# Performance work log

Measured on AMD Instinct MI355X. Metric: run time of the kernel, lower is better.

The kernel has to match this reference:

```python
import jax, jax.numpy as jnp
import numpy as np

B, A, HR = 2, 180, 512
H_OUT = W_OUT = 512


def setup_inputs() -> dict:
    key = jax.random.key(0)
    k1, = jax.random.split(key, 1)
    sino = jax.random.normal(k1, (B, A, HR), dtype=jnp.float32)
    angles_deg = jnp.linspace(0.0, 180.0, A, endpoint=False, dtype=jnp.float32)
    return {"sino": sino, "angles_deg": angles_deg, "H": H_OUT, "W": W_OUT}


def _forward(sino, angles_deg, H, W):
    Bn, An, Hr = sino.shape
    pad = int(1.0 * 0.1 * min(H, W))  # pad_ratio = 1.0
    Hp, Wp = H + 2 * pad, W + 2 * pad

    # --- F.interpolate bilinear, align_corners=False: (A,B,Hr,1) -> (A,B,Hp,Wp).
    # Input width is 1, so width interp replicates the single column; only height interp matters.
    src = jnp.clip((jnp.arange(Hp, dtype=jnp.float32) + 0.5) * (Hr / Hp) - 0.5, 0.0, Hr - 1)
    i0 = jnp.floor(src).astype(jnp.int32)
    i1 = jnp.minimum(i0 + 1, Hr - 1)
    wH = src - i0.astype(jnp.float32)
    p = jnp.transpose(sino, (1, 0, 2)).astype(jnp.float32)  # (A,B,Hr)
    col = p[:, :, i0] * (1.0 - wH) + p[:, :, i1] * wH       # (A,B,Hp)
    proj = jnp.broadcast_to(col[:, :, :, None], (An, Bn, Hp, Wp))  # (A,B,Hp,Wp)

    # --- affine_grid (align_corners=False), sign = -1
    th = -jnp.deg2rad(angles_deg)
    c, s = jnp.cos(th), jnp.sin(th)                          # (A,)
    xs = (jnp.arange(Wp, dtype=jnp.float32) + 0.5) * (2.0 / Wp) - 1.0
    ys = (jnp.arange(Hp, dtype=jnp.float32) + 0.5) * (2.0 / Hp) - 1.0
    gx = c[:, None, None] * xs[None, None, :] - s[:, None, None] * ys[None, :, None]  # (A,Hp,Wp)
    gy = s[:, None, None] * xs[None, None, :] + c[:, None, None] * ys[None, :, None]

    # --- grid_sample bilinear, zeros padding, align_corners=False
    ix = ((gx + 1.0) * Wp - 1.0) * 0.5
    iy = ((gy + 1.0) * Hp - 1.0) * 0.5
    x0 = jnp.floor(ix).astype(jnp.int32); x1 = x0 + 1
    y0 = jnp.floor(iy).astype(jnp.int32); y1 = y0 + 1
    wx = ix - x0.astype(jnp.float32)
    wy = iy - y0.astype(jnp.float32)

    def corner(img, xi, yi, w):  # img (B,Hp,Wp); idx/w (Hp,Wp)
        valid = (xi >= 0) & (xi <= Wp - 1) & (yi >= 0) & (yi <= Hp - 1)
        xc = jnp.clip(xi, 0, Wp - 1)
        yc = jnp.clip(yi, 0, Hp - 1)
        return img[:, yc, xc] * (w * valid.astype(jnp.float32))[None]

    def sample(img, x0a, x1a, y0a, y1a, wxa, wya):
        return (corner(img, x0a, y0a, (1 - wxa) * (1 - wya)) +
                corner(img, x1a, y0a, wxa * (1 - wya)) +
                corner(img, x0a, y1a, (1 - wxa) * wya) +
                corner(img, x1a, y1a, wxa * wya))

    xr = jax.vmap(sample)(proj, x0, x1, y0, y1, wx, wy)      # (A,B,Hp,Wp)
    acc = xr.sum(axis=0) / (An + 1e-06)                      # (B,Hp,Wp)
    acc = acc[:, None, :, :]                                 # (B,1,Hp,Wp)
    if pad > 0:
        acc = acc[:, :, pad:Hp - pad, pad:Wp - pad]
    return acc


def reference(sino, angles_deg, H, W):
    return _forward(sino, angles_deg, H, W)
```

## Files before the change

### kernel.cpp

```cpp
#include <hip/hip_runtime.h>
#include <hip/hip_fp16.h>
#include <math.h>

#define B_N   2
#define A_N   180
#define HR_N  512
#define H_OUT 512
#define W_OUT 512
#define PAD   51
#define HP    614
#define WP    614
#define GUARD 80
#define HPP   (HP + 2*GUARD)
#define NPIX  (H_OUT * W_OUT)

#define TW    16
#define TH    16
#define QA    45
#define CH_Q  15
#define NCH   3
#define WIN   24
#define CHUNK_E (4 * CH_Q * WIN)


__device__ __forceinline__ float col_val(const float* __restrict__ sino,
                                         int b, int a, int yy) {
    if (yy < 0 || yy >= HP) return 0.0f;
    float src = ((float)yy + 0.5f) * ((float)HR_N / (float)HP) - 0.5f;
    src = fminf(fmaxf(src, 0.0f), (float)(HR_N - 1));
    int i0 = (int)floorf(src);
    int i1 = min(i0 + 1, HR_N - 1);
    float wH = src - (float)i0;
    const float* srow = sino + ((size_t)b * A_N + a) * HR_N;
    return srow[i0] * (1.0f - wH) + srow[i1] * wH;
}

__global__ void prep_kernel(const float* __restrict__ sino,
                            const float* __restrict__ angles,
                            uint2* __restrict__ pk2,
                            float2* __restrict__ tg) {
    int idx = blockIdx.x * blockDim.x + threadIdx.x;
    if (idx < A_N) {
        float th = -angles[idx] * (float)(M_PI / 180.0);
        tg[idx] = make_float2(cosf(th), sinf(th));
    }
    const int total = A_N * HPP;
    if (idx < total) {
        int y = idx % HPP;
        int a = idx / HPP;
        int yy = y - GUARD;
        float v00 = col_val(sino, 0, a, yy);
        float v10 = col_val(sino, 1, a, yy);
        float v01 = col_val(sino, 0, a, yy + 1);
        float v11 = col_val(sino, 1, a, yy + 1);
        __half2 lo = __floats2half2_rn(v00, v10);
        __half2 hi = __floats2half2_rn(v01, v11);
        uint2 u;
        u.x = *(unsigned int*)&lo;
        u.y = *(unsigned int*)&hi;
        pk2[idx] = u;
    }
}

__device__ __forceinline__ __half2 interp(uint2 cv, float w) {
    __half2 lo = *(__half2*)&cv.x, hi = *(__half2*)&cv.y;
    return __hfma2(__float2half2_rn(w), __hsub2(hi, lo), lo);
}

template <bool INTERIOR>
__device__ __forceinline__ void bp_body(const uint2* __restrict__ pk2,
                                        const float4* __restrict__ s_cs,
                                        uint2* __restrict__ s_win,
                                        int t, int q, float X, float Y,
                                        float& p00, float& p01, float& p10, float& p11,
                                        float& q00, float& q01, float& q10, float& q11) {
    for (int ch = 0; ch < NCH; ++ch) {
        for (int e = t; e < CHUNK_E; e += 256) {
            int wid = e / WIN;
            int j   = e - wid * WIN;
            int qq  = wid / CH_Q;
            int la  = wid - qq * CH_Q;
            int a   = qq * QA + ch * CH_Q + la;
            s_win[e] = pk2[__float_as_uint(s_cs[a].w) + (unsigned)j];
        }
        __syncthreads();

        const int abase = q * QA + ch * CH_Q;
        const int wbase = q * (CH_Q * WIN);
        if (INTERIOR) {
            __half2 h00 = __float2half2_rn(0.0f);
            __half2 h01 = __float2half2_rn(0.0f);
            __half2 h10 = __float2half2_rn(0.0f);
            __half2 h11 = __float2half2_rn(0.0f);
#pragma unroll
            for (int la = 0; la < CH_Q; ++la) {
                float4 cs = s_cs[abase + la];
                float c = cs.x, s = cs.y;
                float f00 = fmaf(s, X, fmaf(c, Y, cs.z));
                float f01 = f00 + s;
                float f10 = f00 + 8.0f * c;
                float f11 = f10 + s;
                int i00 = (int)f00;  float w00 = __builtin_amdgcn_fractf(f00);
                int i01 = (int)f01;  float w01 = __builtin_amdgcn_fractf(f01);
                int i10 = (int)f10;  float w10 = __builtin_amdgcn_fractf(f10);
                int i11 = (int)f11;  float w11 = __builtin_amdgcn_fractf(f11);
                const int wb = wbase + la * WIN;
                uint2 v00 = s_win[wb + i00];
                uint2 v01 = s_win[wb + i01];
                uint2 v10 = s_win[wb + i10];
                uint2 v11 = s_win[wb + i11];
                h00 = __hadd2(h00, interp(v00, w00));
                h01 = __hadd2(h01, interp(v01, w01));
                h10 = __hadd2(h10, interp(v10, w10));
                h11 = __hadd2(h11, interp(v11, w11));
            }
            p00 += __low2float(h00);  p01 += __high2float(h00);
            p10 += __low2float(h01);  p11 += __high2float(h01);
            q00 += __low2float(h10);  q01 += __high2float(h10);
            q10 += __low2float(h11);  q11 += __high2float(h11);
        } else {
#pragma unroll
            for (int la = 0; la < CH_Q; ++la) {
                float4 cs = s_cs[abase + la];
                float c = cs.x, s = cs.y;
                float f00 = fmaf(s, X, fmaf(c, Y, cs.z));
                float f01 = f00 + s;
                float f10 = f00 + 8.0f * c;
                float f11 = f10 + s;
                int i00 = (int)f00;  float w00 = __builtin_amdgcn_fractf(f00);
                int i01 = (int)f01;  float w01 = __builtin_amdgcn_fractf(f01);
                int i10 = (int)f10;  float w10 = __builtin_amdgcn_fractf(f10);
                int i11 = (int)f11;  float w11 = __builtin_amdgcn_fractf(f11);
                const int wb = wbase + la * WIN;
                __half2 r00 = interp(s_win[wb + i00], w00);
                __half2 r01 = interp(s_win[wb + i01], w01);
                __half2 r10 = interp(s_win[wb + i10], w10);
                __half2 r11 = interp(s_win[wb + i11], w11);
                float ix00 = fmaf(c, X, fmaf(-s, Y, 306.5f));
                float ix01 = ix00 + c;
                float ix10 = ix00 - 8.0f * s;
                float ix11 = ix10 + c;
                float xf00 = fminf(fmaxf(ix00 + 1.0f, 0.0f), 1.0f)
                           * fminf(fmaxf((float)WP - ix00, 0.0f), 1.0f);
                float xf01 = fminf(fmaxf(ix01 + 1.0f, 0.0f), 1.0f)
                           * fminf(fmaxf((float)WP - ix01, 0.0f), 1.0f);
                float xf10 = fminf(fmaxf(ix10 + 1.0f, 0.0f), 1.0f)
                           * fminf(fmaxf((float)WP - ix10, 0.0f), 1.0f);
                float xf11 = fminf(fmaxf(ix11 + 1.0f, 0.0f), 1.0f)
                           * fminf(fmaxf((float)WP - ix11, 0.0f), 1.0f);
                p00 = fmaf(xf00, __low2float(r00),  p00);
                p01 = fmaf(xf00, __high2float(r00), p01);
                p10 = fmaf(xf01, __low2float(r01),  p10);
                p11 = fmaf(xf01, __high2float(r01), p11);
                q00 = fmaf(xf10, __low2float(r10),  q00);
                q01 = fmaf(xf10, __high2float(r10), q01);
                q10 = fmaf(xf11, __low2float(r11),  q10);
                q11 = fmaf(xf11, __high2float(r11), q11);
            }
        }
        __syncthreads();
    }
}

__global__ __launch_bounds__(256, 4) void bp_kernel(const uint2* __restrict__ pk2,
                                                    const float2* __restrict__ tgv,
                                                    float* __restrict__ out) {
    __shared__ float4 s_cs[A_N];
    __shared__ uint2  s_win[CHUNK_E];
    __shared__ float  s_red[3 * 64 * 9];

    int t  = threadIdx.x;
    int tx = blockIdx.x, ty = blockIdx.y;
    float Xc = (float)(tx * TW) - 248.0f;
    float Yc = (float)(ty * TH) - 248.0f;

    if (t < A_N) {
        float2 cs = tgv[t];
        float iyc = fmaf(cs.y, Xc, fmaf(cs.x, Yc, 306.5f));
        int base = (int)floorf(iyc) - 11;
        s_cs[t] = make_float4(cs.x, cs.y, 306.5f - (float)base,
                              __uint_as_float((unsigned)(t * HPP + GUARD + base)));
    }

    int q  = t >> 6;
    int tt = t & 63;
    int lx = (tt & 7) << 1;
    int ly = tt >> 3;
    float X = (float)(tx * TW + lx) - 255.5f;
    float Y = (float)(ty * TH + ly) - 255.5f;

    float p00 = 0.0f, p01 = 0.0f, p10 = 0.0f, p11 = 0.0f;
    float q00 = 0.0f, q01 = 0.0f, q10 = 0.0f, q11 = 0.0f;
    __syncthreads();

    bool interior = (Xc * Xc + Yc * Yc) <= 87500.0f;
    if (interior)
        bp_body<true >(pk2, s_cs, s_win, t, q, X, Y, p00, p01, p10, p11, q00, q01, q10, q11);
    else
        bp_body<false>(pk2, s_cs, s_win, t, q, X, Y, p00, p01, p10, p11, q00, q01, q10, q11);

    if (q != 0) {
        float* r = &s_red[((q - 1) * 64 + tt) * 9];
        r[0] = p00; r[1] = p01; r[2] = p10; r[3] = p11;
        r[4] = q00; r[5] = q01; r[6] = q10; r[7] = q11;
    }
    __syncthreads();
    if (q == 0) {
        const float inv = 1.0f / (180.0f + 1e-6f);
        const float* r0 = &s_red[tt * 9];
        const float* r1 = &s_red[(64 + tt) * 9];
        const float* r2 = &s_red[(128 + tt) * 9];
        int col  = tx * TW + lx;
        int idx0 = (ty * TH + ly) * W_OUT + col;
        int idx1 = idx0 + 8 * W_OUT;
        float2 o;
        o.x = (p00 + r0[0] + r1[0] + r2[0]) * inv;
        o.y = (p10 + r0[2] + r1[2] + r2[2]) * inv;
        *(float2*)(out + idx0) = o;
        o.x = (p01 + r0[1] + r1[1] + r2[1]) * inv;
        o.y = (p11 + r0[3] + r1[3] + r2[3]) * inv;
        *(float2*)(out + NPIX + idx0) = o;
        o.x = (q00 + r0[4] + r1[4] + r2[4]) * inv;
        o.y = (q10 + r0[6] + r1[6] + r2[6]) * inv;
        *(float2*)(out + idx1) = o;
        o.x = (q01 + r0[5] + r1[5] + r2[5]) * inv;
        o.y = (q11 + r0[7] + r1[7] + r2[7]) * inv;
        *(float2*)(out + NPIX + idx1) = o;
    }
}

extern "C" void kernel_launch(void* const* d_in, const int* in_sizes, int n_in,
                              void* d_out, int out_size, void* d_ws, size_t ws_size,
                              hipStream_t stream) {
    const float* sino   = (const float*)d_in[0];
    const float* angles = (const float*)d_in[1];
    char*   ws  = (char*)d_ws;
    uint2*  pk2 = (uint2*)ws;
    float2* tg  = (float2*)(ws + (size_t)A_N * HPP * sizeof(uint2));

    const int total = A_N * HPP;
    prep_kernel<<<(total + 255) / 256, 256, 0, stream>>>(sino, angles, pk2, tg);

    dim3 grid(W_OUT / TW, H_OUT / TH);
    bp_kernel<<<grid, 256, 0, stream>>>(pk2, tg, (float*)d_out);
}
```

Before: 82.42 us.

## Fuse prep kernel into backprojection, computing packed column entries on the fly

Removes the separate prep kernel that precomputed the interpolated, half-packed sinogram columns and the trig table. The backprojection kernel now computes cos/sin per block and builds each shared-memory window entry directly from the raw sinogram, with four interpolated loads per entry. This drops one launch and the round trip through the workspace buffer, at the cost of redundant interpolation and transcendental work in every block. The window fill becomes more arithmetic- and gather-heavy.

```diff
diff --git a/kernel.cpp b/kernel.cpp
--- a/kernel.cpp
+++ b/kernel.cpp
@@ -10,8 +10,6 @@
 #define PAD   51
 #define HP    614
 #define WP    614
-#define GUARD 80
-#define HPP   (HP + 2*GUARD)
 #define NPIX  (H_OUT * W_OUT)
 
 #define TW    16
@@ -35,40 +33,27 @@
     return srow[i0] * (1.0f - wH) + srow[i1] * wH;
 }
 
-__global__ void prep_kernel(const float* __restrict__ sino,
-                            const float* __restrict__ angles,
-                            uint2* __restrict__ pk2,
-                            float2* __restrict__ tg) {
-    int idx = blockIdx.x * blockDim.x + threadIdx.x;
-    if (idx < A_N) {
-        float th = -angles[idx] * (float)(M_PI / 180.0);
-        tg[idx] = make_float2(cosf(th), sinf(th));
-    }
-    const int total = A_N * HPP;
-    if (idx < total) {
-        int y = idx % HPP;
-        int a = idx / HPP;
-        int yy = y - GUARD;
-        float v00 = col_val(sino, 0, a, yy);
-        float v10 = col_val(sino, 1, a, yy);
-        float v01 = col_val(sino, 0, a, yy + 1);
-        float v11 = col_val(sino, 1, a, yy + 1);
-        __half2 lo = __floats2half2_rn(v00, v10);
-        __half2 hi = __floats2half2_rn(v01, v11);
-        uint2 u;
-        u.x = *(unsigned int*)&lo;
-        u.y = *(unsigned int*)&hi;
-        pk2[idx] = u;
-    }
-}
-
 __device__ __forceinline__ __half2 interp(uint2 cv, float w) {
     __half2 lo = *(__half2*)&cv.x, hi = *(__half2*)&cv.y;
     return __hfma2(__float2half2_rn(w), __hsub2(hi, lo), lo);
 }
 
+__device__ __forceinline__ uint2 make_entry(const float* __restrict__ sino,
+                                            int a, int yy) {
+    float v00 = col_val(sino, 0, a, yy);
+    float v10 = col_val(sino, 1, a, yy);
+    float v01 = col_val(sino, 0, a, yy + 1);
+    float v11 = col_val(sino, 1, a, yy + 1);
+    __half2 lo = __floats2half2_rn(v00, v10);
+    __half2 hi = __floats2half2_rn(v01, v11);
+    uint2 u;
+    u.x = *(unsigned int*)&lo;
+    u.y = *(unsigned int*)&hi;
+    return u;
+}
+
 template <bool INTERIOR>
-__device__ __forceinline__ void bp_body(const uint2* __restrict__ pk2,
+__device__ __forceinline__ void bp_body(const float* __restrict__ sino,
                                         const float4* __restrict__ s_cs,
                                         uint2* __restrict__ s_win,
                                         int t, int q, float X, float Y,
@@ -81,7 +66,8 @@
             int qq  = wid / CH_Q;
             int la  = wid - qq * CH_Q;
             int a   = qq * QA + ch * CH_Q + la;
-            s_win[e] = pk2[__float_as_uint(s_cs[a].w) + (unsigned)j];
+            int yy  = __float_as_int(s_cs[a].w) + j;
+            s_win[e] = make_entry(sino, a, yy);
         }
         __syncthreads();
 
@@ -162,9 +148,9 @@
     }
 }
 
-__global__ __launch_bounds__(256, 4) void bp_kernel(const uint2* __restrict__ pk2,
-                                                    const float2* __restrict__ tgv,
-                                                    float* __restrict__ out) {
+__global__ __launch_bounds__(256, 4) void bp_fused(const float* __restrict__ sino,
+                                                   const float* __restrict__ angles,
+                                                   float* __restrict__ out) {
     __shared__ float4 s_cs[A_N];
     __shared__ uint2  s_win[CHUNK_E];
     __shared__ float  s_red[3 * 64 * 9];
@@ -175,11 +161,12 @@
     float Yc = (float)(ty * TH) - 248.0f;
 
     if (t < A_N) {
-        float2 cs = tgv[t];
-        float iyc = fmaf(cs.y, Xc, fmaf(cs.x, Yc, 306.5f));
+        float th = -angles[t] * (float)(M_PI / 180.0);
+        float c  = cosf(th);
+        float s  = sinf(th);
+        float iyc = fmaf(s, Xc, fmaf(c, Yc, 306.5f));
         int base = (int)floorf(iyc) - 11;
-        s_cs[t] = make_float4(cs.x, cs.y, 306.5f - (float)base,
-                              __uint_as_float((unsigned)(t * HPP + GUARD + base)));
+        s_cs[t] = make_float4(c, s, 306.5f - (float)base, __int_as_float(base));
     }
 
     int q  = t >> 6;
@@ -195,9 +182,9 @@
 
     bool interior = (Xc * Xc + Yc * Yc) <= 87500.0f;
     if (interior)
-        bp_body<true >(pk2, s_cs, s_win, t, q, X, Y, p00, p01, p10, p11, q00, q01, q10, q11);
+        bp_body<true >(sino, s_cs, s_win, t, q, X, Y, p00, p01, p10, p11, q00, q01, q10, q11);
     else
-        bp_body<false>(pk2, s_cs, s_win, t, q, X, Y, p00, p01, p10, p11, q00, q01, q10, q11);
+        bp_body<false>(sino, s_cs, s_win, t, q, X, Y, p00, p01, p10, p11, q00, q01, q10, q11);
 
     if (q != 0) {
         float* r = &s_red[((q - 1) * 64 + tt) * 9];
@@ -234,13 +221,8 @@
                               hipStream_t stream) {
     const float* sino   = (const float*)d_in[0];
     const float* angles = (const float*)d_in[1];
-    char*   ws  = (char*)d_ws;
-    uint2*  pk2 = (uint2*)ws;
-    float2* tg  = (float2*)(ws + (size_t)A_N * HPP * sizeof(uint2));
-
-    const int total = A_N * HPP;
-    prep_kernel<<<(total + 255) / 256, 256, 0, stream>>>(sino, angles, pk2, tg);
+    (void)d_ws; (void)ws_size;
 
     dim3 grid(W_OUT / TW, H_OUT / TH);
-    bp_kernel<<<grid, 256, 0, stream>>>(pk2, tg, (float*)d_out);
-}
+    bp_fused<<<grid, 256, 0, stream>>>(sino, angles, (float*)d_out);
+}
```

New measurement: 91.27 us. 1.11x slower.
